# Kernel tuning notes

Measured on AMD Instinct MI355X. Metric: run time of the kernel, lower is better.

Reference implementation:

```python
import jax, jax.numpy as jnp
import numpy as np

PASS = 8        # pass_through_size
FLOW = 16       # flow_size
TRANS = FLOW - PASS  # transform_size = 8
NBINS = 64
HID = 1024


def _conditioner(yA, w1, b1, w2, b2, w3, b3):
    # MLP producing unnormalized positive bin widths Q: [B, TRANS, NBINS]
    h = jax.nn.relu(yA @ w1 + b1)
    h = jax.nn.relu(h @ w2 + b2)
    q = jax.nn.softplus(h @ w3 + b3) + 1e-6  # positivity for slopes
    return q.reshape(-1, TRANS, NBINS)


def setup_inputs() -> dict:
    key = jax.random.key(0)
    ks = jax.random.split(key, 4)
    B = 65536
    y = jax.random.uniform(ks[0], (B, FLOW + 1), dtype=jnp.float32)
    w1 = jax.random.normal(ks[1], (PASS, HID), dtype=jnp.float32) / np.sqrt(PASS)
    w2 = jax.random.normal(ks[2], (HID, HID), dtype=jnp.float32) / np.sqrt(HID)
    w3 = jax.random.normal(ks[3], (HID, TRANS * NBINS), dtype=jnp.float32) / np.sqrt(HID)
    return {
        "y": y,
        "w1": w1, "b1": jnp.zeros((HID,), jnp.float32),
        "w2": w2, "b2": jnp.zeros((HID,), jnp.float32),
        "w3": w3, "b3": jnp.zeros((TRANS * NBINS,), jnp.float32),
    }


def reference(y, w1, b1, w2, b2, w3, b3):
    yA = y[:, :PASS]                      # [B, PASS]
    yB = y[:, PASS:FLOW]                  # [B, TRANS]
    jac = y[:, FLOW:FLOW + 1]             # [B, 1]

    Q = _conditioner(yA, w1, b1, w2, b2, w3, b3)  # [B, TRANS, NBINS]
    Qsum = jnp.cumsum(Q, axis=-1)
    Qnorms = Qsum[:, :, -1:]
    Q = Q / (Qnorms / NBINS)              # slopes per bin
    Qsum = Qsum / Qnorms                  # normalized CDF knots (last == 1)

    # searchsorted(side='left') per row: count of knots strictly below value
    ybins = jnp.sum(Qsum < yB[..., None], axis=-1)          # [B, TRANS] int32
    ybins = jnp.clip(ybins, 0, NBINS - 1)                   # guard fp edge case

    paddedQsum = jnp.pad(Qsum, ((0, 0), (0, 0), (1, 0)))    # prepend 0 knot
    offsets = jnp.take_along_axis(paddedQsum, ybins[..., None], axis=-1)[..., 0]
    slopes = jnp.take_along_axis(Q, ybins[..., None], axis=-1)[..., 0]

    xB = (yB - offsets) / slopes + ybins.astype(jnp.float32) / NBINS
    jac = jac * jnp.prod(1.0 / slopes, axis=-1, keepdims=True)
    return jnp.concatenate((yA, xB, jac), axis=-1)          # [B, FLOW+1]
```

## Files before the change

kernel.cpp:

```cpp
#include <hip/hip_runtime.h>
#include <hip/hip_fp16.h>

#define HID 1024
#define QCOLS 512
#define KP 2048
#define NT 48

typedef _Float16 f16x8 __attribute__((ext_vector_type(8)));
typedef float f32x4 __attribute__((ext_vector_type(4)));

__global__ void tconv_both(const float* __restrict__ w2, __half* __restrict__ w2t,
                           const float* __restrict__ w3, __half* __restrict__ w3t) {
  __shared__ float tile[32][33];
  const int z = blockIdx.z;
  const int N = z ? QCOLS : HID;
  if (blockIdx.x * 32 >= N) return;
  const float* src = z ? w3 : w2;
  __half* dst = z ? w3t : w2t;
  int n0 = blockIdx.x * 32, k0 = blockIdx.y * 32;
  int tx = threadIdx.x, ty = threadIdx.y;
  for (int i = ty; i < 32; i += 8)
    tile[i][tx] = src[(size_t)(k0 + i) * N + n0 + tx];
  __syncthreads();
  for (int i = ty; i < 32; i += 8) {
    float v = tile[tx][i] * 256.f;
    __half h = __float2half(v);
    size_t o = (size_t)(n0 + i) * KP + k0 + tx;
    dst[o] = h;
    dst[o + 1024] = __float2half(v - __half2float(h));
  }
}

__global__ __launch_bounds__(256)
void h1k(const float* __restrict__ y, const float* __restrict__ w1,
         const float* __restrict__ b1, __half* __restrict__ h1,
         int row0, int nrows) {
  const int t = threadIdx.x & 127;
  const int rl = threadIdx.x >> 7;
  const long r = (long)blockIdx.x * 2 + rl;
  if (r >= nrows) return;
  const float* yr = y + (size_t)(row0 + r) * 17;
  float yv[8];
#pragma unroll
  for (int k = 0; k < 8; ++k) yv[k] = yr[k];
  const int c0 = t * 8;
  f32x4 a0 = *(const f32x4*)(b1 + c0);
  f32x4 a1 = *(const f32x4*)(b1 + c0 + 4);
#pragma unroll
  for (int k = 0; k < 8; ++k) {
    const f32x4 w0 = *(const f32x4*)(w1 + k * HID + c0);
    const f32x4 w1v = *(const f32x4*)(w1 + k * HID + c0 + 4);
#pragma unroll
    for (int j = 0; j < 4; ++j) {
      a0[j] = fmaf(yv[k], w0[j], a0[j]);
      a1[j] = fmaf(yv[k], w1v[j], a1[j]);
    }
  }
  f16x8 hi, lo;
#pragma unroll
  for (int j = 0; j < 8; ++j) {
    float v = fmaxf(j < 4 ? a0[j] : a1[j - 4], 0.f) * 64.f;
    _Float16 h = (_Float16)v;
    hi[j] = h;
    lo[j] = (_Float16)(v - (float)h);
  }
  *(f16x8*)(h1 + (size_t)r * KP + c0) = hi;
  *(f16x8*)(h1 + (size_t)r * KP + c0 + 1024) = lo;
}

template <int ACT>
__device__ __forceinline__
void gemm8p_body(const __half* __restrict__ A, const __half* __restrict__ B,
                 const float* __restrict__ bias, __half* __restrict__ Co,
                 float* __restrict__ Cf, int ldc) {
  __shared__ char lds[131072];
  const int tid = threadIdx.x;
  const int lane = tid & 63, wave = tid >> 6;
  const int p = lane & 15, ql = lane >> 4;
  const int wm = wave >> 2, wn = wave & 3;

  const int gx = gridDim.x, nwg = gx * gridDim.y;
  const int bid = blockIdx.y * gx + blockIdx.x;
  const int q8 = nwg >> 3, r8 = nwg & 7;
  const int xcd = bid & 7, lxi = bid >> 3;
  const int swz = (xcd < r8 ? xcd * (q8 + 1) : r8 * (q8 + 1) + (xcd - r8) * q8) + lxi;
  const size_t row_blk = (size_t)(swz / gx) * 256;
  const size_t col_blk = (size_t)(swz % gx) * 256;

  int a_off[8], b_off[4];
#pragma unroll
  for (int m = 0; m < 8; ++m) {
    int r = wm * 128 + m * 16 + p;
    a_off[m] = r * 64 + ((ql ^ ((r >> 1) & 3)) << 4);
  }
#pragma unroll
  for (int n = 0; n < 4; ++n) {
    int r = wn * 64 + n * 16 + p;
    b_off[n] = r * 64 + ((ql ^ ((r >> 1) & 3)) << 4);
  }

  const int idx0 = tid, idx1 = tid + 512;
  const int sr0 = idx0 >> 2, sq0 = (idx0 & 3) ^ ((sr0 >> 1) & 3);
  const int sr1 = idx1 >> 2, sq1 = (idx1 & 3) ^ ((sr1 >> 1) & 3);

  auto stage = [&](int buf, int h, int kt) {
    const int lk = kt * 64;
    const int ak = ((lk >= 2048) ? 1024 : 0) + (lk & 1023) + h * 32;
    const int bk = ((lk >= 1024 && lk < 2048) ? 1024 : 0) + (lk & 1023) + h * 32;
    char* pa = lds + buf * 65536 + h * 16384;
    char* pb = pa + 32768;
    const __half* ga0 = A + (row_blk + sr0) * (size_t)KP + ak + sq0 * 8;
    const __half* ga1 = A + (row_blk + sr1) * (size_t)KP + ak + sq1 * 8;
    const __half* gb0 = B + (col_blk + sr0) * (size_t)KP + bk + sq0 * 8;
    const __half* gb1 = B + (col_blk + sr1) * (size_t)KP + bk + sq1 * 8;
    __builtin_amdgcn_global_load_lds((__attribute__((address_space(1))) void*)ga0,
        (__attribute__((address_space(3))) void*)(pa + idx0 * 16), 16, 0, 0);
    __builtin_amdgcn_global_load_lds((__attribute__((address_space(1))) void*)ga1,
        (__attribute__((address_space(3))) void*)(pa + idx1 * 16), 16, 0, 0);
    __builtin_amdgcn_global_load_lds((__attribute__((address_space(1))) void*)gb0,
        (__attribute__((address_space(3))) void*)(pb + idx0 * 16), 16, 0, 0);
    __builtin_amdgcn_global_load_lds((__attribute__((address_space(1))) void*)gb1,
        (__attribute__((address_space(3))) void*)(pb + idx1 * 16), 16, 0, 0);
  };

  stage(0, 0, 0);
  stage(0, 1, 0);
  asm volatile("s_waitcnt vmcnt(0)" ::: "memory");
  __builtin_amdgcn_s_barrier();

  f32x4 acc[8][4] = {};

  for (int t = 0; t < NT; ++t) {
    const int bufp = t & 1;
    const int ts = (t + 1 < NT) ? t + 1 : NT - 1;
#pragma unroll
    for (int h = 0; h < 2; ++h) {
      const char* pA = lds + bufp * 65536 + h * 16384;
      const char* pB = pA + 32768;
      f16x8 af[8], bfr[4];
#pragma unroll
      for (int m = 0; m < 8; ++m) af[m] = *(const f16x8*)(pA + a_off[m]);
#pragma unroll
      for (int n = 0; n < 4; ++n) bfr[n] = *(const f16x8*)(pB + b_off[n]);
      stage(bufp ^ 1, h, ts);
      __builtin_amdgcn_sched_barrier(0);
      __builtin_amdgcn_s_barrier();
      __builtin_amdgcn_sched_barrier(0);
      __builtin_amdgcn_s_setprio(1);
#pragma unroll
      for (int m = 0; m < 8; ++m)
#pragma unroll
        for (int n = 0; n < 4; ++n)
          acc[m][n] = __builtin_amdgcn_mfma_f32_16x16x32_f16(af[m], bfr[n], acc[m][n], 0, 0, 0);
      __builtin_amdgcn_s_setprio(0);
      asm volatile("s_waitcnt vmcnt(4)" ::: "memory");
      __builtin_amdgcn_sched_barrier(0);
      __builtin_amdgcn_s_barrier();
      __builtin_amdgcn_sched_barrier(0);
    }
  }

  const float unscale = 1.f / 16384.f;
#pragma unroll
  for (int n = 0; n < 4; ++n) {
    const size_t col = col_blk + wn * 64 + n * 16 + p;
    const float bv = bias[col];
#pragma unroll
    for (int m = 0; m < 8; ++m) {
      const size_t row0 = row_blk + wm * 128 + m * 16 + ql * 4;
#pragma unroll
      for (int j = 0; j < 4; ++j) {
        float v = acc[m][n][j] * unscale + bv;
        const size_t o = (row0 + j) * (size_t)ldc + col;
        if constexpr (ACT == 0) {
          float r = fmaxf(v, 0.f) * 64.f;
          __half hh = __float2half(r);
          Co[o] = hh;
          Co[o + 1024] = __float2half(r - __half2float(hh));
        } else {
          float sp = fmaxf(v, 0.f) + log1pf(expf(-fabsf(v)));
          Cf[o] = sp + 1e-6f;
        }
      }
    }
  }
}

__global__ __launch_bounds__(512, 2)
void g2relu(const __half* __restrict__ A, const __half* __restrict__ B,
            const float* __restrict__ bias, __half* __restrict__ Co) {
  gemm8p_body<0>(A, B, bias, Co, nullptr, KP);
}

__global__ __launch_bounds__(512, 2)
void g3soft(const __half* __restrict__ A, const __half* __restrict__ B,
            const float* __restrict__ bias, float* __restrict__ Cf) {
  gemm8p_body<1>(A, B, bias, nullptr, Cf, QCOLS);
}

__global__ __launch_bounds__(256)
void pwl_epi(const float* __restrict__ y, const float* __restrict__ q,
             float* __restrict__ out, int row0, int nrows) {
  const int wave = threadIdx.x >> 6, lane = threadIdx.x & 63;
  const int r = blockIdx.x * 4 + wave;
  if (r >= nrows) return;
  const float* yr = y + (size_t)(row0 + r) * 17;
  float* orow = out + (size_t)(row0 + r) * 17;
  const float* qr = q + (size_t)r * QCOLS;
  float prod_inv = 1.f;
#pragma unroll
  for (int t = 0; t < 8; ++t) {
    const float qv = qr[t * 64 + lane];
    float s = qv;
#pragma unroll
    for (int d = 1; d < 64; d <<= 1) {
      float u = __shfl_up(s, d);
      if (lane >= d) s += u;
    }
    const float total = __shfl(s, 63);
    const float sn = s / total;
    const float dnorm = total * 0.015625f;
    const float slope_l = qv / dnorm;
    const float yb = yr[8 + t];
    const unsigned long long m = __ballot(sn < yb);
    int bin = (int)__popcll(m);
    bin = bin > 63 ? 63 : bin;
    const float off_g = __shfl(sn, bin > 0 ? bin - 1 : 0);
    const float off = (bin == 0) ? 0.f : off_g;
    const float sl = __shfl(slope_l, bin);
    const float xB = (yb - off) / sl + (float)bin * 0.015625f;
    if (lane == t) orow[8 + t] = xB;
    prod_inv *= (1.f / sl);
  }
  if (lane < 8) orow[lane] = yr[lane];
  if (lane == 8) orow[16] = yr[16] * prod_inv;
}

extern "C" void kernel_launch(void* const* d_in, const int* in_sizes, int n_in,
                              void* d_out, int out_size, void* d_ws, size_t ws_size,
                              hipStream_t stream) {
  const float* y  = (const float*)d_in[0];
  const float* w1 = (const float*)d_in[1];
  const float* b1 = (const float*)d_in[2];
  const float* w2 = (const float*)d_in[3];
  const float* b2 = (const float*)d_in[4];
  const float* w3 = (const float*)d_in[5];
  const float* b3 = (const float*)d_in[6];
  float* out = (float*)d_out;
  const long Btot = in_sizes[0] / 17;

  char* ws = (char*)d_ws;
  __half* w2t = (__half*)ws;
  __half* w3t = (__half*)(ws + (4u << 20));
  const size_t fixed = (size_t)6 << 20;

  const size_t avail = ws_size > fixed ? ws_size - fixed : 0;
  long maxrows = (long)(avail / 8192);
  long chunk = 256;
  for (long c = 65536; c >= 256; c >>= 1) {
    if (c <= maxrows && c <= Btot) { chunk = c; break; }
  }

  __half* h1buf = (__half*)(ws + fixed);
  __half* h2buf = (__half*)(ws + fixed + (size_t)chunk * 4096);
  float* qbuf = (float*)h1buf;

  tconv_both<<<dim3(32, 32, 2), dim3(32, 8), 0, stream>>>(w2, w2t, w3, w3t);

  for (long row0 = 0; row0 < Btot; row0 += chunk) {
    const int nr = (int)((Btot - row0 < chunk) ? (Btot - row0) : chunk);
    h1k<<<(nr + 1) / 2, 256, 0, stream>>>(y, w1, b1, h1buf, (int)row0, nr);
    g2relu<<<dim3(HID / 256, nr / 256), 512, 0, stream>>>(h1buf, w2t, b2, h2buf);
    g3soft<<<dim3(QCOLS / 256, nr / 256), 512, 0, stream>>>(h2buf, w3t, b3, qbuf);
    pwl_epi<<<(nr + 3) / 4, 256, 0, stream>>>(y, qbuf, out, (int)row0, nr);
  }
}
```

Before: 1.082 ms.

## Use four-slot LDS ring pipeline in GEMMs and narrow third GEMM tile

Replaces the double-buffered half-step staging with a four-slot ring buffer in LDS that keeps three K-phases in flight. The wait is relaxed to a vmcnt that still allows outstanding loads, which should hide more global latency. The third GEMM now uses a 256x128 tile, doubling its workgroup count for better CU occupancy on the small N=512 output. The cost is re-reading the A tile more often in the third GEMM and a tighter LDS and vmcnt accounting that must be exactly right.

```diff
diff --git a/kernel.cpp b/kernel.cpp
--- a/kernel.cpp
+++ b/kernel.cpp
@@ -68,12 +68,16 @@
   *(f16x8*)(h1 + (size_t)r * KP + c0 + 1024) = lo;
 }
 
-template <int ACT>
+template <int ACT, int BN>
 __device__ __forceinline__
-void gemm8p_body(const __half* __restrict__ A, const __half* __restrict__ B,
-                 const float* __restrict__ bias, __half* __restrict__ Co,
-                 float* __restrict__ Cf, int ldc) {
-  __shared__ char lds[131072];
+void gemm_ring_body(const __half* __restrict__ A, const __half* __restrict__ Bt,
+                    const float* __restrict__ bias, __half* __restrict__ Co,
+                    float* __restrict__ Cf, int ldc) {
+  constexpr int NFRAG = BN / 64;
+  constexpr int BNB = BN * 64;
+  constexpr int SLOT = 16384 + BNB;
+  constexpr int LPS = 2 + BN / 128;
+  __shared__ char lds[4 * SLOT];
   const int tid = threadIdx.x;
   const int lane = tid & 63, wave = tid >> 6;
   const int p = lane & 15, ql = lane >> 4;
@@ -85,17 +89,17 @@
   const int xcd = bid & 7, lxi = bid >> 3;
   const int swz = (xcd < r8 ? xcd * (q8 + 1) : r8 * (q8 + 1) + (xcd - r8) * q8) + lxi;
   const size_t row_blk = (size_t)(swz / gx) * 256;
-  const size_t col_blk = (size_t)(swz % gx) * 256;
-
-  int a_off[8], b_off[4];
+  const size_t col_blk = (size_t)(swz % gx) * BN;
+
+  int a_off[8], b_off[NFRAG];
 #pragma unroll
   for (int m = 0; m < 8; ++m) {
     int r = wm * 128 + m * 16 + p;
     a_off[m] = r * 64 + ((ql ^ ((r >> 1) & 3)) << 4);
   }
 #pragma unroll
-  for (int n = 0; n < 4; ++n) {
-    int r = wn * 64 + n * 16 + p;
+  for (int n = 0; n < NFRAG; ++n) {
+    int r = wn * (BN / 4) + n * 16 + p;
     b_off[n] = r * 64 + ((ql ^ ((r >> 1) & 3)) << 4);
   }
 
@@ -103,67 +107,66 @@
   const int sr0 = idx0 >> 2, sq0 = (idx0 & 3) ^ ((sr0 >> 1) & 3);
   const int sr1 = idx1 >> 2, sq1 = (idx1 & 3) ^ ((sr1 >> 1) & 3);
 
-  auto stage = [&](int buf, int h, int kt) {
+  auto gload = [&](const __half* g, char* l) {
+    __builtin_amdgcn_global_load_lds((__attribute__((address_space(1))) void*)g,
+        (__attribute__((address_space(3))) void*)l, 16, 0, 0);
+  };
+
+  auto stage = [&](int q) {
+    int kt = q >> 1; if (kt > NT - 1) kt = NT - 1;
+    const int h = q & 1;
     const int lk = kt * 64;
     const int ak = ((lk >= 2048) ? 1024 : 0) + (lk & 1023) + h * 32;
     const int bk = ((lk >= 1024 && lk < 2048) ? 1024 : 0) + (lk & 1023) + h * 32;
-    char* pa = lds + buf * 65536 + h * 16384;
-    char* pb = pa + 32768;
-    const __half* ga0 = A + (row_blk + sr0) * (size_t)KP + ak + sq0 * 8;
-    const __half* ga1 = A + (row_blk + sr1) * (size_t)KP + ak + sq1 * 8;
-    const __half* gb0 = B + (col_blk + sr0) * (size_t)KP + bk + sq0 * 8;
-    const __half* gb1 = B + (col_blk + sr1) * (size_t)KP + bk + sq1 * 8;
-    __builtin_amdgcn_global_load_lds((__attribute__((address_space(1))) void*)ga0,
-        (__attribute__((address_space(3))) void*)(pa + idx0 * 16), 16, 0, 0);
-    __builtin_amdgcn_global_load_lds((__attribute__((address_space(1))) void*)ga1,
-        (__attribute__((address_space(3))) void*)(pa + idx1 * 16), 16, 0, 0);
-    __builtin_amdgcn_global_load_lds((__attribute__((address_space(1))) void*)gb0,
-        (__attribute__((address_space(3))) void*)(pb + idx0 * 16), 16, 0, 0);
-    __builtin_amdgcn_global_load_lds((__attribute__((address_space(1))) void*)gb1,
-        (__attribute__((address_space(3))) void*)(pb + idx1 * 16), 16, 0, 0);
+    char* base = lds + (q & 3) * SLOT;
+    char* pb = base + 16384;
+    gload(A + (row_blk + sr0) * (size_t)KP + ak + sq0 * 8, base + idx0 * 16);
+    gload(A + (row_blk + sr1) * (size_t)KP + ak + sq1 * 8, base + idx1 * 16);
+    gload(Bt + (col_blk + sr0) * (size_t)KP + bk + sq0 * 8, pb + idx0 * 16);
+    if constexpr (BN == 256)
+      gload(Bt + (col_blk + sr1) * (size_t)KP + bk + sq1 * 8, pb + idx1 * 16);
   };
 
-  stage(0, 0, 0);
-  stage(0, 1, 0);
-  asm volatile("s_waitcnt vmcnt(0)" ::: "memory");
+  auto wait_ring = [&]() {
+    if constexpr (LPS == 4) asm volatile("s_waitcnt vmcnt(8)" ::: "memory");
+    else                    asm volatile("s_waitcnt vmcnt(6)" ::: "memory");
+  };
+
+  stage(0); stage(1); stage(2);
+  wait_ring();
   __builtin_amdgcn_s_barrier();
 
-  f32x4 acc[8][4] = {};
-
-  for (int t = 0; t < NT; ++t) {
-    const int bufp = t & 1;
-    const int ts = (t + 1 < NT) ? t + 1 : NT - 1;
-#pragma unroll
-    for (int h = 0; h < 2; ++h) {
-      const char* pA = lds + bufp * 65536 + h * 16384;
-      const char* pB = pA + 32768;
-      f16x8 af[8], bfr[4];
-#pragma unroll
-      for (int m = 0; m < 8; ++m) af[m] = *(const f16x8*)(pA + a_off[m]);
-#pragma unroll
-      for (int n = 0; n < 4; ++n) bfr[n] = *(const f16x8*)(pB + b_off[n]);
-      stage(bufp ^ 1, h, ts);
-      __builtin_amdgcn_sched_barrier(0);
-      __builtin_amdgcn_s_barrier();
-      __builtin_amdgcn_sched_barrier(0);
-      __builtin_amdgcn_s_setprio(1);
-#pragma unroll
-      for (int m = 0; m < 8; ++m)
-#pragma unroll
-        for (int n = 0; n < 4; ++n)
-          acc[m][n] = __builtin_amdgcn_mfma_f32_16x16x32_f16(af[m], bfr[n], acc[m][n], 0, 0, 0);
-      __builtin_amdgcn_s_setprio(0);
-      asm volatile("s_waitcnt vmcnt(4)" ::: "memory");
-      __builtin_amdgcn_sched_barrier(0);
-      __builtin_amdgcn_s_barrier();
-      __builtin_amdgcn_sched_barrier(0);
-    }
+  f32x4 acc[8][NFRAG] = {};
+
+  for (int ph = 0; ph < NT * 2; ++ph) {
+    const char* base = lds + (ph & 3) * SLOT;
+    const char* pB = base + 16384;
+    f16x8 af[8], bfr[NFRAG];
+#pragma unroll
+    for (int m = 0; m < 8; ++m) af[m] = *(const f16x8*)(base + a_off[m]);
+#pragma unroll
+    for (int n = 0; n < NFRAG; ++n) bfr[n] = *(const f16x8*)(pB + b_off[n]);
+    stage(ph + 3);
+    __builtin_amdgcn_sched_barrier(0);
+    __builtin_amdgcn_s_barrier();
+    __builtin_amdgcn_sched_barrier(0);
+    __builtin_amdgcn_s_setprio(1);
+#pragma unroll
+    for (int m = 0; m < 8; ++m)
+#pragma unroll
+      for (int n = 0; n < NFRAG; ++n)
+        acc[m][n] = __builtin_amdgcn_mfma_f32_16x16x32_f16(af[m], bfr[n], acc[m][n], 0, 0, 0);
+    __builtin_amdgcn_s_setprio(0);
+    wait_ring();
+    __builtin_amdgcn_sched_barrier(0);
+    __builtin_amdgcn_s_barrier();
+    __builtin_amdgcn_sched_barrier(0);
   }
 
   const float unscale = 1.f / 16384.f;
 #pragma unroll
-  for (int n = 0; n < 4; ++n) {
-    const size_t col = col_blk + wn * 64 + n * 16 + p;
+  for (int n = 0; n < NFRAG; ++n) {
+    const size_t col = col_blk + wn * (BN / 4) + n * 16 + p;
     const float bv = bias[col];
 #pragma unroll
     for (int m = 0; m < 8; ++m) {
@@ -189,13 +192,13 @@
 __global__ __launch_bounds__(512, 2)
 void g2relu(const __half* __restrict__ A, const __half* __restrict__ B,
             const float* __restrict__ bias, __half* __restrict__ Co) {
-  gemm8p_body<0>(A, B, bias, Co, nullptr, KP);
+  gemm_ring_body<0, 256>(A, B, bias, Co, nullptr, KP);
 }
 
 __global__ __launch_bounds__(512, 2)
 void g3soft(const __half* __restrict__ A, const __half* __restrict__ B,
             const float* __restrict__ bias, float* __restrict__ Cf) {
-  gemm8p_body<1>(A, B, bias, nullptr, Cf, QCOLS);
+  gemm_ring_body<1, 128>(A, B, bias, nullptr, Cf, QCOLS);
 }
 
 __global__ __launch_bounds__(256)
@@ -271,7 +274,7 @@
     const int nr = (int)((Btot - row0 < chunk) ? (Btot - row0) : chunk);
     h1k<<<(nr + 1) / 2, 256, 0, stream>>>(y, w1, b1, h1buf, (int)row0, nr);
     g2relu<<<dim3(HID / 256, nr / 256), 512, 0, stream>>>(h1buf, w2t, b2, h2buf);
-    g3soft<<<dim3(QCOLS / 256, nr / 256), 512, 0, stream>>>(h2buf, w3t, b3, qbuf);
+    g3soft<<<dim3(QCOLS / 128, nr / 256), 512, 0, stream>>>(h2buf, w3t, b3, qbuf);
     pwl_epi<<<(nr + 3) / 4, 256, 0, stream>>>(y, qbuf, out, (int)row0, nr);
   }
 }
```

New measurement: 913.4 us. 15.6% less time.
